# Kernel optimization log

Measured on AMD Instinct MI355X. Metric: run time of the kernel, lower is better.

Reference implementation:

```python
import jax, jax.numpy as jnp
import numpy as np
from jax import lax

B, T, V = 32, 2048, 32  # batch, num observations (frames), state vocabulary


def setup_inputs() -> dict:
    key = jax.random.key(0)
    k1, k2, k3, k4, k5 = jax.random.split(key, 5)
    inputs = jax.random.normal(k1, (B, T, V, V), dtype=jnp.float32)
    targets = jax.random.randint(k2, (B, T + 1), 0, V)  # state sequence z_0..z_T
    transition = 0.1 * jax.random.normal(k3, (V, V), dtype=jnp.float32)
    initial = 0.1 * jax.random.normal(k4, (V,), dtype=jnp.float32)
    final = 0.1 * jax.random.normal(k5, (V,), dtype=jnp.float32)
    return {"inputs": inputs, "transition": transition, "initial": initial,
            "final": final, "targets": targets}


def _log_prob(inputs, transition, initial, final, targets):
    # inputs: [B,T,V,V] arc scores score[b,t,i,j] for transition i->j at step t
    # Lattice semantics (compose(obs_fst, seq_fst)): a path is z_0..z_T with
    #   weight = initial[z_0] + sum_t (score[t, z_t, z_{t+1}] + A[z_t, z_{t+1}]) + final[z_T]
    b, t = inputs.shape[0], inputs.shape[1]
    v = transition.shape[0]

    # ---- denominator: forward algorithm (log-sum-exp DP over the lattice) ----
    scores_t = jnp.transpose(inputs, (1, 0, 2, 3))  # [T,B,V,V]
    alpha0 = jnp.broadcast_to(initial[None, :], (b, v))  # [B,V]

    def step(alpha, s_t):
        # alpha: [B,V] over previous state i; s_t: [B,V,V]
        m = alpha[:, :, None] + s_t + transition[None, :, :]  # [B,V,V]
        return jax.nn.logsumexp(m, axis=1), None

    alphaT, _ = lax.scan(step, alpha0, scores_t)
    denom = jax.nn.logsumexp(alphaT + final[None, :], axis=-1)  # [B]

    # ---- numerator: score of the ground-truth path ----
    y_prev = targets[:, :-1]  # [B,T]
    y_next = targets[:, 1:]   # [B,T]
    flat = inputs.reshape(b, t, v * v)
    emit = jnp.take_along_axis(flat, (y_prev * v + y_next)[..., None], axis=2)[..., 0]  # [B,T]
    trans = transition[y_prev, y_next]  # [B,T]
    num = (initial[targets[:, 0]]
           + jnp.sum(emit + trans, axis=1)
           + final[targets[:, -1]])  # [B]

    return num - denom  # log p(targets | inputs), per sequence: [B]


def reference(inputs, transition, initial, final, targets):
    return _log_prob(inputs, transition, initial, final, targets)
```

## Files before the change

### kernel.cpp

```cpp
#include <hip/hip_runtime.h>
#include <hip/hip_bf16.h>
#include <cmath>

#define Bz 32
#define Tz 2048
#define Vz 32
#define Cz 64
#define Lz 32
#define WPB 4

typedef short short8 __attribute__((ext_vector_type(8)));
typedef float f32x16 __attribute__((ext_vector_type(16)));
typedef float f32x4  __attribute__((ext_vector_type(4)));

static __device__ __forceinline__ unsigned short f2bf(float x) {
    unsigned u = __builtin_bit_cast(unsigned, x);
    u += 0x7FFFu + ((u >> 16) & 1u);
    return (unsigned short)(u >> 16);
}

static __device__ __forceinline__ void gl_lds16(const float* g, float* l) {
    __builtin_amdgcn_global_load_lds(
        (const __attribute__((address_space(1))) void*)g,
        (__attribute__((address_space(3))) void*)l, 16, 0, 0);
}

__global__ void __launch_bounds__(256) crf_chunks(
    const float* __restrict__ inputs, const float* __restrict__ trans,
    const int* __restrict__ targets, float* __restrict__ Pout,
    float* __restrict__ numpart)
{
    __shared__ __align__(16) float trans_lds[1024];
    __shared__ __align__(16) float sbuf[WPB][3 * 1024];
    __shared__ __align__(16) unsigned short elds[WPB][32 * 40];
    __shared__ __align__(16) float cbuf[WPB][32];

    const int tid  = threadIdx.x;
    const int lane = tid & 63;
    const int wid  = tid >> 6;
    const int gid  = __builtin_amdgcn_readfirstlane(blockIdx.x * WPB + wid);
    const int b    = gid >> 6;
    const int c    = gid & (Cz - 1);

    const int h = lane >> 5;
    const int j = lane & 31;
    const int kbase = 8 * h;

    float tr[16];
#pragma unroll
    for (int e = 0; e < 8; ++e) {
        tr[e]     = trans[(kbase + e) * Vz + j];
        tr[8 + e] = trans[(16 + kbase + e) * Vz + j];
    }

    ((float4*)trans_lds)[tid] = ((const float4*)trans)[tid];
    __syncthreads();

    const float* src = inputs + ((size_t)b * Tz + (size_t)c * Lz) * (Vz * Vz);
    const int*   tgb = targets + b * (Tz + 1) + c * Lz;
    int tgv = (lane < Lz + 1) ? tgb[lane] : 0;

    float* sw = sbuf[wid];
    {
        const float* g0 = src + lane * 4;
#pragma unroll
        for (int q = 0; q < 4; ++q) gl_lds16(g0 + q * 256, sw + q * 256);
        const float* g1 = src + 1024 + lane * 4;
#pragma unroll
        for (int q = 0; q < 4; ++q) gl_lds16(g1 + q * 256, sw + 1024 + q * 256);
    }

    f32x16 p;
    float cj = 0.f;
    float epart = 0.f;
    float ckr[16];
#pragma unroll
    for (int e = 0; e < 16; ++e) ckr[e] = 0.f;

    for (int t = 0; t < Lz; ++t) {
        if (t + 2 < Lz) {
            const float* g = src + (t + 2) * 1024 + lane * 4;
            float* dst = sw + ((t + 2) % 3) * 1024;
#pragma unroll
            for (int q = 0; q < 4; ++q) gl_lds16(g + q * 256, dst + q * 256);
        }
        const int rem = Lz - 1 - t;
        if (rem >= 2)      { asm volatile("s_waitcnt vmcnt(8)" ::: "memory"); }
        else if (rem == 1) { asm volatile("s_waitcnt vmcnt(4)" ::: "memory"); }
        else               { asm volatile("s_waitcnt vmcnt(0)" ::: "memory"); }
        __builtin_amdgcn_sched_barrier(0);

        const float* sb = sw + (t % 3) * 1024;

        {
            int yp = __shfl(tgv, t, 64);
            int yn = __shfl(tgv, t + 1, 64);
            int eidx = yp * Vz + yn;
            epart += sb[eidx] + trans_lds[eidx];
        }

        float m[16];
#pragma unroll
        for (int e = 0; e < 8; ++e) {
            m[e]     = sb[(kbase + e) * Vz + j]      + tr[e]     + ckr[e];
            m[8 + e] = sb[(16 + kbase + e) * Vz + j] + tr[8 + e] + ckr[8 + e];
        }
        float d = m[0];
#pragma unroll
        for (int e = 1; e < 16; ++e) d = fmaxf(d, m[e]);
        d = fmaxf(d, __shfl_xor(d, 32, 64));

        short8 B1, B2;
#pragma unroll
        for (int e = 0; e < 8; ++e) {
            B1[e] = (short)f2bf(__expf(m[e] - d));
            B2[e] = (short)f2bf(__expf(m[8 + e] - d));
        }

        short8 A1, A2;
        if (t == 0) {
#pragma unroll
            for (int e = 0; e < 8; ++e) {
                A1[e] = (short)((kbase + e == j) ? 0x3F80 : 0);
                A2[e] = (short)((16 + kbase + e == j) ? 0x3F80 : 0);
            }
        } else {
            const unsigned short* ew = elds[wid] + j * 40;
            A1 = *(const short8*)(ew + kbase);
            A2 = *(const short8*)(ew + 16 + kbase);
        }

        f32x16 z = {};
        p = __builtin_amdgcn_mfma_f32_32x32x16_bf16(A1, B1, z, 0, 0, 0);
        p = __builtin_amdgcn_mfma_f32_32x32x16_bf16(A2, B2, p, 0, 0, 0);

        float mj = p[0];
#pragma unroll
        for (int r = 1; r < 16; ++r) mj = fmaxf(mj, p[r]);
        mj = fmaxf(mj, __shfl_xor(mj, 32, 64));
        float inv = 1.0f / mj;
#pragma unroll
        for (int r = 0; r < 16; ++r) p[r] *= inv;
        cj = d + __logf(mj);

        unsigned short* ew = elds[wid];
#pragma unroll
        for (int r = 0; r < 16; ++r) {
            const int row = (r & 3) + 8 * (r >> 2) + 4 * h;
            ew[row * 40 + j] = f2bf(p[r]);
        }
        if (lane < 32) cbuf[wid][j] = cj;
        {
            const float* cb = cbuf[wid];
            f32x4 c0 = *(const f32x4*)(cb + kbase);
            f32x4 c1 = *(const f32x4*)(cb + kbase + 4);
            f32x4 c2 = *(const f32x4*)(cb + 16 + kbase);
            f32x4 c3 = *(const f32x4*)(cb + 16 + kbase + 4);
#pragma unroll
            for (int v = 0; v < 4; ++v) {
                ckr[v] = c0[v]; ckr[4 + v] = c1[v];
                ckr[8 + v] = c2[v]; ckr[12 + v] = c3[v];
            }
        }
    }

    float* Pc = Pout + (size_t)gid * 1024;
#pragma unroll
    for (int r = 0; r < 16; ++r) {
        const int row = (r & 3) + 8 * (r >> 2) + 4 * h;
        Pc[row * Vz + j] = cj + __logf(p[r]);
    }
    if (lane == 0) numpart[gid] = epart;
}

#define LOADQ(buf, chunk)                                                  \
    do { if ((chunk) < Cz) {                                               \
        const float* Pn = Pb + (size_t)(chunk) * 1024;                     \
        _Pragma("unroll")                                                  \
        for (int ii = 0; ii < 16; ++ii) buf[ii] = Pn[(hh + ii) * 32 + j];  \
    } } while (0)

#define PROCQ(buf)                                                         \
    do {                                                                   \
        float x[16];                                                       \
        _Pragma("unroll")                                                  \
        for (int ii = 0; ii < 16; ++ii)                                    \
            x[ii] = __shfl(al, hh + ii, 64) + buf[ii];                     \
        float u0 = fmaxf(x[0], x[1]),  u1 = fmaxf(x[2], x[3]);             \
        float u2 = fmaxf(x[4], x[5]),  u3 = fmaxf(x[6], x[7]);             \
        float u4 = fmaxf(x[8], x[9]),  u5 = fmaxf(x[10], x[11]);           \
        float u6 = fmaxf(x[12], x[13]), u7 = fmaxf(x[14], x[15]);          \
        u0 = fmaxf(u0, u1); u2 = fmaxf(u2, u3);                            \
        u4 = fmaxf(u4, u5); u6 = fmaxf(u6, u7);                            \
        u0 = fmaxf(u0, u2); u4 = fmaxf(u4, u6);                            \
        float mx = fmaxf(u0, u4);                                          \
        mx = fmaxf(mx, __shfl_xor(mx, 32, 64));                            \
        float e[16];                                                       \
        _Pragma("unroll")                                                  \
        for (int ii = 0; ii < 16; ++ii) e[ii] = __expf(x[ii] - mx);        \
        float s0 = e[0] + e[1],   s1 = e[2] + e[3];                        \
        float s2 = e[4] + e[5],   s3 = e[6] + e[7];                        \
        float s4 = e[8] + e[9],   s5 = e[10] + e[11];                      \
        float s6 = e[12] + e[13], s7 = e[14] + e[15];                      \
        s0 += s1; s2 += s3; s4 += s5; s6 += s7;                            \
        s0 += s2; s4 += s6;                                                \
        float s = s0 + s4;                                                 \
        s += __shfl_xor(s, 32, 64);                                        \
        al = mx + __logf(s);                                               \
    } while (0)

__global__ void __launch_bounds__(64) crf_combine(
    const float* __restrict__ Pout, const float* __restrict__ numpart,
    const float* __restrict__ initial, const float* __restrict__ fin,
    const int* __restrict__ targets, float* __restrict__ out)
{
    const int lane = threadIdx.x;
    const int b = blockIdx.x;
    const int h = lane >> 5;
    const int j = lane & 31;
    const int hh = h * 16;

    const float* Pb = Pout + (size_t)b * Cz * 1024;
    float al = initial[j];

    float q0[16], q1[16], q2[16], q3[16];
    LOADQ(q0, 0); LOADQ(q1, 1); LOADQ(q2, 2); LOADQ(q3, 3);

    for (int cc = 0; cc < Cz; cc += 4) {
        PROCQ(q0); LOADQ(q0, cc + 4);
        PROCQ(q1); LOADQ(q1, cc + 5);
        PROCQ(q2); LOADQ(q2, cc + 6);
        PROCQ(q3); LOADQ(q3, cc + 7);
    }

    float mm = (h == 0) ? (al + fin[j]) : -INFINITY;
    float ss = 1.f;
#pragma unroll
    for (int off = 32; off >= 1; off >>= 1) {
        float om = __shfl_xor(mm, off, 64);
        float os = __shfl_xor(ss, off, 64);
        float nm = fmaxf(mm, om);
        ss = ss * __expf(mm - nm) + os * __expf(om - nm);
        mm = nm;
    }
    float denom = mm + __logf(ss);

    float np = numpart[b * Cz + lane];
#pragma unroll
    for (int off = 32; off >= 1; off >>= 1) np += __shfl_xor(np, off, 64);

    if (lane == 0) {
        const int* tg = targets + b * (Tz + 1);
        out[b] = np + initial[tg[0]] + fin[tg[Tz]] - denom;
    }
}

extern "C" void kernel_launch(void* const* d_in, const int* in_sizes, int n_in,
                              void* d_out, int out_size, void* d_ws, size_t ws_size,
                              hipStream_t stream) {
    const float* inputs  = (const float*)d_in[0];
    const float* trans   = (const float*)d_in[1];
    const float* initial = (const float*)d_in[2];
    const float* fin     = (const float*)d_in[3];
    const int*   targets = (const int*)d_in[4];

    float* Pout    = (float*)d_ws;
    float* numpart = Pout + (size_t)Bz * Cz * 1024;

    hipLaunchKernelGGL(crf_chunks, dim3(Bz * Cz / WPB), dim3(256), 0, stream,
                       inputs, trans, targets, Pout, numpart);
    hipLaunchKernelGGL(crf_combine, dim3(Bz), dim3(64), 0, stream,
                       Pout, numpart, initial, fin, targets, (float*)d_out);
}
```

Measured before the change: 406.0 us.

## Restructure chunk kernel: register prefetch, transposed MFMA, global-max scaling, lazy renorm

The chunk kernel no longer stages inputs through LDS with async global-to-LDS loads. It loads scores straight into registers with a four-step prefetch ring and swaps the MFMA operand roles, so the propagated P matrix is repacked into bf16 with lane shuffles instead of an LDS round-trip. Per-column shifts are replaced by one wave-wide max shift, accumulated in a scalar, and P is renormalised only every fourth step. This removes LDS traffic and per-step syncs. It risks bf16 underflow from the coarser scaling and adds register pressure; the combine kernel also switches to float4 loads, which reads P as its transpose.

Result: no change. 400.1 us (-1.4%).

```diff
diff --git a/kernel.cpp b/kernel.cpp
--- a/kernel.cpp
+++ b/kernel.cpp
@@ -1,5 +1,4 @@
 #include <hip/hip_runtime.h>
-#include <hip/hip_bf16.h>
 #include <cmath>
 
 #define Bz 32
@@ -11,203 +10,177 @@
 
 typedef short short8 __attribute__((ext_vector_type(8)));
 typedef float f32x16 __attribute__((ext_vector_type(16)));
-typedef float f32x4  __attribute__((ext_vector_type(4)));
-
-static __device__ __forceinline__ unsigned short f2bf(float x) {
+typedef unsigned int u32x4 __attribute__((ext_vector_type(4)));
+
+static __device__ __forceinline__ unsigned f2bf_u(float x) {
     unsigned u = __builtin_bit_cast(unsigned, x);
     u += 0x7FFFu + ((u >> 16) & 1u);
-    return (unsigned short)(u >> 16);
-}
-
-static __device__ __forceinline__ void gl_lds16(const float* g, float* l) {
-    __builtin_amdgcn_global_load_lds(
-        (const __attribute__((address_space(1))) void*)g,
-        (__attribute__((address_space(3))) void*)l, 16, 0, 0);
-}
-
-__global__ void __launch_bounds__(256) crf_chunks(
+    return u >> 16;
+}
+static __device__ __forceinline__ unsigned cvtpk(float lo, float hi) {
+    unsigned r;
+    asm("v_cvt_pk_bf16_f32 %0, %1, %2" : "=v"(r) : "v"(lo), "v"(hi));
+    return r;
+}
+
+#define WMAX16(dst, arr) do {                                               \
+    float w0=fmaxf(arr[0],arr[1]),  w1=fmaxf(arr[2],arr[3]);                \
+    float w2=fmaxf(arr[4],arr[5]),  w3=fmaxf(arr[6],arr[7]);                \
+    float w4=fmaxf(arr[8],arr[9]),  w5=fmaxf(arr[10],arr[11]);              \
+    float w6=fmaxf(arr[12],arr[13]),w7=fmaxf(arr[14],arr[15]);              \
+    w0=fmaxf(w0,w1); w2=fmaxf(w2,w3); w4=fmaxf(w4,w5); w6=fmaxf(w6,w7);     \
+    w0=fmaxf(w0,w2); w4=fmaxf(w4,w6); dst = fmaxf(w0,w4);                   \
+} while (0)
+
+#define WAVEMAXF(v) do {                                                    \
+    v = fmaxf(v, __shfl_xor(v, 1, 64));                                     \
+    v = fmaxf(v, __shfl_xor(v, 2, 64));                                     \
+    v = fmaxf(v, __shfl_xor(v, 4, 64));                                     \
+    v = fmaxf(v, __shfl_xor(v, 8, 64));                                     \
+    v = fmaxf(v, __shfl_xor(v, 16, 64));                                    \
+    v = fmaxf(v, __shfl_xor(v, 32, 64));                                    \
+} while (0)
+
+__global__ void __launch_bounds__(256, 2) crf_chunks(
     const float* __restrict__ inputs, const float* __restrict__ trans,
     const int* __restrict__ targets, float* __restrict__ Pout,
     float* __restrict__ numpart)
 {
     __shared__ __align__(16) float trans_lds[1024];
-    __shared__ __align__(16) float sbuf[WPB][3 * 1024];
-    __shared__ __align__(16) unsigned short elds[WPB][32 * 40];
-    __shared__ __align__(16) float cbuf[WPB][32];
 
     const int tid  = threadIdx.x;
     const int lane = tid & 63;
     const int wid  = tid >> 6;
-    const int gid  = __builtin_amdgcn_readfirstlane(blockIdx.x * WPB + wid);
+    const int gid  = blockIdx.x * WPB + wid;
     const int b    = gid >> 6;
     const int c    = gid & (Cz - 1);
 
-    const int h = lane >> 5;
-    const int j = lane & 31;
-    const int kbase = 8 * h;
+    const int H   = lane >> 5;
+    const int col = lane & 31;
+    const int kb1 = 8 * H;
+    const int kb2 = 16 + 8 * H;
 
     float tr[16];
 #pragma unroll
     for (int e = 0; e < 8; ++e) {
-        tr[e]     = trans[(kbase + e) * Vz + j];
-        tr[8 + e] = trans[(16 + kbase + e) * Vz + j];
-    }
-
+        tr[e]     = trans[(kb1 + e) * Vz + col];
+        tr[8 + e] = trans[(kb2 + e) * Vz + col];
+    }
     ((float4*)trans_lds)[tid] = ((const float4*)trans)[tid];
     __syncthreads();
 
-    const float* src = inputs + ((size_t)b * Tz + (size_t)c * Lz) * (Vz * Vz);
-    const int*   tgb = targets + b * (Tz + 1) + c * Lz;
-    int tgv = (lane < Lz + 1) ? tgb[lane] : 0;
-
-    float* sw = sbuf[wid];
-    {
-        const float* g0 = src + lane * 4;
-#pragma unroll
-        for (int q = 0; q < 4; ++q) gl_lds16(g0 + q * 256, sw + q * 256);
-        const float* g1 = src + 1024 + lane * 4;
-#pragma unroll
-        for (int q = 0; q < 4; ++q) gl_lds16(g1 + q * 256, sw + 1024 + q * 256);
+    const float* src = inputs + ((size_t)b * Tz + (size_t)c * Lz) * 1024;
+
+    const int* tgb = targets + b * (Tz + 1) + c * Lz;
+    int tg  = (lane <= Lz) ? tgb[lane] : 0;
+    int tgn = __shfl(tg, lane + 1, 64);
+    float epart = 0.f;
+    if (lane < Lz) {
+        int eidx = tg * Vz + tgn;
+        epart = src[lane * 1024 + eidx] + trans_lds[eidx];
     }
 
     f32x16 p;
-    float cj = 0.f;
-    float epart = 0.f;
-    float ckr[16];
-#pragma unroll
-    for (int e = 0; e < 16; ++e) ckr[e] = 0.f;
-
-    for (int t = 0; t < Lz; ++t) {
-        if (t + 2 < Lz) {
-            const float* g = src + (t + 2) * 1024 + lane * 4;
-            float* dst = sw + ((t + 2) % 3) * 1024;
-#pragma unroll
-            for (int q = 0; q < 4; ++q) gl_lds16(g + q * 256, dst + q * 256);
-        }
-        const int rem = Lz - 1 - t;
-        if (rem >= 2)      { asm volatile("s_waitcnt vmcnt(8)" ::: "memory"); }
-        else if (rem == 1) { asm volatile("s_waitcnt vmcnt(4)" ::: "memory"); }
-        else               { asm volatile("s_waitcnt vmcnt(0)" ::: "memory"); }
-        __builtin_amdgcn_sched_barrier(0);
-
-        const float* sb = sw + (t % 3) * 1024;
-
-        {
-            int yp = __shfl(tgv, t, 64);
-            int yn = __shfl(tgv, t + 1, 64);
-            int eidx = yp * Vz + yn;
-            epart += sb[eidx] + trans_lds[eidx];
-        }
-
-        float m[16];
-#pragma unroll
-        for (int e = 0; e < 8; ++e) {
-            m[e]     = sb[(kbase + e) * Vz + j]      + tr[e]     + ckr[e];
-            m[8 + e] = sb[(16 + kbase + e) * Vz + j] + tr[8 + e] + ckr[8 + e];
-        }
-        float d = m[0];
-#pragma unroll
-        for (int e = 1; e < 16; ++e) d = fmaxf(d, m[e]);
-        d = fmaxf(d, __shfl_xor(d, 32, 64));
-
-        short8 B1, B2;
-#pragma unroll
-        for (int e = 0; e < 8; ++e) {
-            B1[e] = (short)f2bf(__expf(m[e] - d));
-            B2[e] = (short)f2bf(__expf(m[8 + e] - d));
-        }
-
-        short8 A1, A2;
-        if (t == 0) {
-#pragma unroll
-            for (int e = 0; e < 8; ++e) {
-                A1[e] = (short)((kbase + e == j) ? 0x3F80 : 0);
-                A2[e] = (short)((16 + kbase + e == j) ? 0x3F80 : 0);
-            }
-        } else {
-            const unsigned short* ew = elds[wid] + j * 40;
-            A1 = *(const short8*)(ew + kbase);
-            A2 = *(const short8*)(ew + 16 + kbase);
-        }
-
-        f32x16 z = {};
-        p = __builtin_amdgcn_mfma_f32_32x32x16_bf16(A1, B1, z, 0, 0, 0);
-        p = __builtin_amdgcn_mfma_f32_32x32x16_bf16(A2, B2, p, 0, 0, 0);
-
-        float mj = p[0];
-#pragma unroll
-        for (int r = 1; r < 16; ++r) mj = fmaxf(mj, p[r]);
-        mj = fmaxf(mj, __shfl_xor(mj, 32, 64));
-        float inv = 1.0f / mj;
-#pragma unroll
-        for (int r = 0; r < 16; ++r) p[r] *= inv;
-        cj = d + __logf(mj);
-
-        unsigned short* ew = elds[wid];
-#pragma unroll
-        for (int r = 0; r < 16; ++r) {
-            const int row = (r & 3) + 8 * (r >> 2) + 4 * h;
-            ew[row * 40 + j] = f2bf(p[r]);
-        }
-        if (lane < 32) cbuf[wid][j] = cj;
-        {
-            const float* cb = cbuf[wid];
-            f32x4 c0 = *(const f32x4*)(cb + kbase);
-            f32x4 c1 = *(const f32x4*)(cb + kbase + 4);
-            f32x4 c2 = *(const f32x4*)(cb + 16 + kbase);
-            f32x4 c3 = *(const f32x4*)(cb + 16 + kbase + 4);
-#pragma unroll
-            for (int v = 0; v < 4; ++v) {
-                ckr[v] = c0[v]; ckr[4 + v] = c1[v];
-                ckr[8 + v] = c2[v]; ckr[12 + v] = c3[v];
-            }
-        }
+#pragma unroll
+    for (int r = 0; r < 16; ++r)
+        p[r] = (((r & 3) + 8 * (r >> 2) + 4 * H) == col) ? 1.f : 0.f;
+    float gam = 0.f;
+
+#define LOADM(buf, t) do {                                                  \
+    const float* s_ = src + (size_t)(t) * 1024;                             \
+    _Pragma("unroll")                                                       \
+    for (int e = 0; e < 8; ++e) {                                           \
+        buf[e]     = s_[(kb1 + e) * Vz + col];                              \
+        buf[8 + e] = s_[(kb2 + e) * Vz + col];                              \
+    } } while (0)
+
+    float mA[16], mB[16], mC[16], mD[16];
+    LOADM(mA, 0); LOADM(mB, 1); LOADM(mC, 2); LOADM(mD, 3);
+
+#define STEP(buf, t, RN) do {                                               \
+    float x[16];                                                            \
+    _Pragma("unroll")                                                       \
+    for (int i_ = 0; i_ < 16; ++i_) x[i_] = buf[i_] + tr[i_];               \
+    if ((t) + 4 < Lz) LOADM(buf, (t) + 4);        \
+    float d; WMAX16(d, x); WAVEMAXF(d);                                     \
+                            \
+    u32x4 a1u, a2u;                                                         \
+    _Pragma("unroll")                                                       \
+    for (int e = 0; e < 4; ++e) {                                           \
+        a1u[e] = f2bf_u(__expf(x[2*e]     - d)) |                           \
+                 (f2bf_u(__expf(x[2*e+1]   - d)) << 16);                    \
+        a2u[e] = f2bf_u(__expf(x[8+2*e]   - d)) |                           \
+                 (f2bf_u(__expf(x[8+2*e+1] - d)) << 16);                    \
+    }                                                                       \
+           \
+    unsigned pk[8], qk[8];                                                  \
+    _Pragma("unroll")                                                       \
+    for (int i_ = 0; i_ < 8; ++i_) pk[i_] = cvtpk(p[2*i_], p[2*i_+1]);      \
+    _Pragma("unroll")                                                       \
+    for (int i_ = 0; i_ < 8; ++i_) qk[i_] = __shfl_xor(pk[i_], 32, 64);     \
+    u32x4 b1u, b2u;                                                         \
+    b1u[0] = H ? qk[2] : pk[0];  b1u[1] = H ? qk[3] : pk[1];                \
+    b1u[2] = H ? pk[2] : qk[0];  b1u[3] = H ? pk[3] : qk[1];                \
+    b2u[0] = H ? qk[6] : pk[4];  b2u[1] = H ? qk[7] : pk[5];                \
+    b2u[2] = H ? pk[6] : qk[4];  b2u[3] = H ? pk[7] : qk[5];                \
+    short8 A1 = __builtin_bit_cast(short8, a1u);                            \
+    short8 A2 = __builtin_bit_cast(short8, a2u);                            \
+    short8 B1 = __builtin_bit_cast(short8, b1u);                            \
+    short8 B2 = __builtin_bit_cast(short8, b2u);                            \
+    f32x16 z = {};                                                          \
+    p = __builtin_amdgcn_mfma_f32_32x32x16_bf16(A1, B1, z, 0, 0, 0);        \
+    p = __builtin_amdgcn_mfma_f32_32x32x16_bf16(A2, B2, p, 0, 0, 0);        \
+    gam += d;                                                               \
+    if (RN) {                                                               \
+        float ms; WMAX16(ms, p); WAVEMAXF(ms);                              \
+        float inv = 1.0f / ms;                                              \
+        _Pragma("unroll")                                                   \
+        for (int r_ = 0; r_ < 16; ++r_) p[r_] *= inv;                       \
+        gam += __logf(ms);                                                  \
+    }                                                                       \
+} while (0)
+
+    for (int t = 0; t < Lz; t += 4) {
+        STEP(mA, t, 0); STEP(mB, t + 1, 0); STEP(mC, t + 2, 0); STEP(mD, t + 3, 1);
     }
 
     float* Pc = Pout + (size_t)gid * 1024;
 #pragma unroll
     for (int r = 0; r < 16; ++r) {
-        const int row = (r & 3) + 8 * (r >> 2) + 4 * h;
-        Pc[row * Vz + j] = cj + __logf(p[r]);
-    }
+        int row = (r & 3) + 8 * (r >> 2) + 4 * H;
+        Pc[row * Vz + col] = gam + __logf(p[r]);
+    }
+#pragma unroll
+    for (int off = 32; off >= 1; off >>= 1) epart += __shfl_xor(epart, off, 64);
     if (lane == 0) numpart[gid] = epart;
 }
 
-#define LOADQ(buf, chunk)                                                  \
-    do { if ((chunk) < Cz) {                                               \
-        const float* Pn = Pb + (size_t)(chunk) * 1024;                     \
-        _Pragma("unroll")                                                  \
-        for (int ii = 0; ii < 16; ++ii) buf[ii] = Pn[(hh + ii) * 32 + j];  \
-    } } while (0)
-
-#define PROCQ(buf)                                                         \
-    do {                                                                   \
-        float x[16];                                                       \
-        _Pragma("unroll")                                                  \
-        for (int ii = 0; ii < 16; ++ii)                                    \
-            x[ii] = __shfl(al, hh + ii, 64) + buf[ii];                     \
-        float u0 = fmaxf(x[0], x[1]),  u1 = fmaxf(x[2], x[3]);             \
-        float u2 = fmaxf(x[4], x[5]),  u3 = fmaxf(x[6], x[7]);             \
-        float u4 = fmaxf(x[8], x[9]),  u5 = fmaxf(x[10], x[11]);           \
-        float u6 = fmaxf(x[12], x[13]), u7 = fmaxf(x[14], x[15]);          \
-        u0 = fmaxf(u0, u1); u2 = fmaxf(u2, u3);                            \
-        u4 = fmaxf(u4, u5); u6 = fmaxf(u6, u7);                            \
-        u0 = fmaxf(u0, u2); u4 = fmaxf(u4, u6);                            \
-        float mx = fmaxf(u0, u4);                                          \
-        mx = fmaxf(mx, __shfl_xor(mx, 32, 64));                            \
-        float e[16];                                                       \
-        _Pragma("unroll")                                                  \
-        for (int ii = 0; ii < 16; ++ii) e[ii] = __expf(x[ii] - mx);        \
-        float s0 = e[0] + e[1],   s1 = e[2] + e[3];                        \
-        float s2 = e[4] + e[5],   s3 = e[6] + e[7];                        \
-        float s4 = e[8] + e[9],   s5 = e[10] + e[11];                      \
-        float s6 = e[12] + e[13], s7 = e[14] + e[15];                      \
-        s0 += s1; s2 += s3; s4 += s5; s6 += s7;                            \
-        s0 += s2; s4 += s6;                                                \
-        float s = s0 + s4;                                                 \
-        s += __shfl_xor(s, 32, 64);                                        \
-        al = mx + __logf(s);                                               \
-    } while (0)
+#define LOADQ(buf, chunk) do { if ((chunk) < Cz) {                          \
+    const float4* Pn = (const float4*)(Pb + (size_t)(chunk) * 1024 + j * 32 + hh); \
+    float4 v0 = Pn[0], v1 = Pn[1], v2 = Pn[2], v3 = Pn[3];                  \
+    buf[0]=v0.x; buf[1]=v0.y; buf[2]=v0.z; buf[3]=v0.w;                     \
+    buf[4]=v1.x; buf[5]=v1.y; buf[6]=v1.z; buf[7]=v1.w;                     \
+    buf[8]=v2.x; buf[9]=v2.y; buf[10]=v2.z; buf[11]=v2.w;                   \
+    buf[12]=v3.x; buf[13]=v3.y; buf[14]=v3.z; buf[15]=v3.w;                 \
+} } while (0)
+
+#define PROCQ(buf) do {                                                     \
+    float x[16];                                                            \
+    _Pragma("unroll")                                                       \
+    for (int ii = 0; ii < 16; ++ii)                                         \
+        x[ii] = __shfl(al, hh + ii, 64) + buf[ii];                          \
+    float mx; WMAX16(mx, x);                                                \
+    mx = fmaxf(mx, __shfl_xor(mx, 32, 64));                                 \
+    float e[16];                                                            \
+    _Pragma("unroll")                                                       \
+    for (int ii = 0; ii < 16; ++ii) e[ii] = __expf(x[ii] - mx);             \
+    float s0=e[0]+e[1],   s1=e[2]+e[3],   s2=e[4]+e[5],   s3=e[6]+e[7];     \
+    float s4=e[8]+e[9],   s5=e[10]+e[11], s6=e[12]+e[13], s7=e[14]+e[15];   \
+    s0+=s1; s2+=s3; s4+=s5; s6+=s7; s0+=s2; s4+=s6;                         \
+    float s = s0 + s4;                                                      \
+    s += __shfl_xor(s, 32, 64);                                             \
+    al = mx + __logf(s);                                                    \
+} while (0)
 
 __global__ void __launch_bounds__(64) crf_combine(
     const float* __restrict__ Pout, const float* __restrict__ numpart,
@@ -225,7 +198,6 @@
 
     float q0[16], q1[16], q2[16], q3[16];
     LOADQ(q0, 0); LOADQ(q1, 1); LOADQ(q2, 2); LOADQ(q3, 3);
-
     for (int cc = 0; cc < Cz; cc += 4) {
         PROCQ(q0); LOADQ(q0, cc + 4);
         PROCQ(q1); LOADQ(q1, cc + 5);
```
